# Performance work log

Hardware: AMD Instinct MI355X
Metric: run time of the kernel (lower is better)

The kernel has to match this reference:

```python
import jax, jax.numpy as jnp
import numpy as np

B, L, C, P, H = 1, 1024, 384, 128, 12
SQK, SV, PQK, PV = 16, 16, 4, 8
DIST_EPS = 1e-8


def setup_inputs() -> dict:
    key = jax.random.key(0)
    ks = jax.random.split(key, 16)
    f32 = jnp.float32
    inputs_1d = jax.random.normal(ks[0], (B, L, C), dtype=f32)
    inputs_2d = jax.random.normal(ks[1], (B, L, L, P), dtype=f32)
    # valid rotation matrices from random unit quaternions
    q = jax.random.normal(ks[2], (B, L, 4), dtype=f32)
    q = q / jnp.linalg.norm(q, axis=-1, keepdims=True)
    w, x, y, z = q[..., 0], q[..., 1], q[..., 2], q[..., 3]
    rotations = jnp.stack([
        jnp.stack([1 - 2 * (y * y + z * z), 2 * (x * y - w * z), 2 * (x * z + w * y)], -1),
        jnp.stack([2 * (x * y + w * z), 1 - 2 * (x * x + z * z), 2 * (y * z - w * x)], -1),
        jnp.stack([2 * (x * z - w * y), 2 * (y * z + w * x), 1 - 2 * (x * x + y * y)], -1)], -2)
    translations = jax.random.normal(ks[3], (B, L, 3), dtype=f32)
    mask = jnp.ones((B, L), dtype=bool)
    s = 0.02  # init scale
    tpw_init = float(np.log(np.exp(1.0) - 1.0))  # softplus^{-1}(1)
    return {
        'inputs_1d': inputs_1d, 'inputs_2d': inputs_2d,
        'rotations': rotations, 'translations': translations, 'mask': mask,
        'Wq': jax.random.normal(ks[4], (C, H * SQK), f32) * s, 'bq': jnp.zeros((H * SQK,), f32),
        'Wkv': jax.random.normal(ks[5], (C, H * (SQK + SV)), f32) * s, 'bkv': jnp.zeros((H * (SQK + SV),), f32),
        'Wqp': jax.random.normal(ks[6], (C, 3 * H * PQK), f32) * s, 'bqp': jnp.zeros((3 * H * PQK,), f32),
        'Wkvp': jax.random.normal(ks[7], (C, 3 * H * (PQK + PV)), f32) * s, 'bkvp': jnp.zeros((3 * H * (PQK + PV),), f32),
        'Wpair': jax.random.normal(ks[8], (P, H), f32) * s, 'bpair': jnp.zeros((H,), f32),
        'tpw': jnp.full((H,), tpw_init, f32),
        'Wout': jax.random.normal(ks[9], (H * (SV + P + PV * 4), C), f32) * s, 'bout': jnp.zeros((C,), f32),
    }


def reference(inputs_1d, inputs_2d, rotations, translations, mask,
              Wq, bq, Wkv, bkv, Wqp, bqp, Wkvp, bkvp, Wpair, bpair, tpw, Wout, bout):
    b, l, _ = inputs_1d.shape
    scalar_w = np.sqrt(1.0 / (3 * SQK))
    point_wc = np.sqrt(1.0 / (3 * PQK * 9.0 / 2))
    pair_w = np.sqrt(1.0 / 3)

    # scalar q/k/v: [b,h,l,c]
    q_s = (inputs_1d @ Wq + bq).reshape(b, l, H, SQK).transpose(0, 2, 1, 3)
    kv_s = (inputs_1d @ Wkv + bkv).reshape(b, l, H, SQK + SV).transpose(0, 2, 1, 3)
    k_s, v_s = kv_s[..., :SQK], kv_s[..., SQK:]
    logits = jnp.einsum('bhic,bhjc->bhij', q_s * scalar_w, k_s)

    def apply_rigid(pts):  # pts: [b,l,n,3] local -> global
        return jnp.einsum('blxy,blny->blnx', rotations, pts) + translations[:, :, None, :]

    # point q/k/v; layout '(r n)' -> [b,l,n,3]
    qp = (inputs_1d @ Wqp + bqp).reshape(b, l, 3, H * PQK).transpose(0, 1, 3, 2)
    qp = apply_rigid(qp).reshape(b, l, H, PQK, 3)  # [b,i,h,n,r]
    kvp = (inputs_1d @ Wkvp + bkvp).reshape(b, l, 3, H * (PQK + PV)).transpose(0, 1, 3, 2)
    kvp = apply_rigid(kvp).reshape(b, l, H, PQK + PV, 3)
    kp, vp = kvp[..., :PQK, :], kvp[..., PQK:, :]

    # squared distances via |q|^2 + |k|^2 - 2 q.k (avoids [b,i,j,h,n,r] blowup)
    qk = jnp.einsum('bihnr,bjhnr->bhij', qp, kp)
    sq_q = jnp.sum(qp * qp, (3, 4)).transpose(0, 2, 1)  # [b,h,i]
    sq_k = jnp.sum(kp * kp, (3, 4)).transpose(0, 2, 1)  # [b,h,j]
    dist2 = sq_q[..., :, None] + sq_k[..., None, :] - 2.0 * qk
    pw = -0.5 * point_wc * jax.nn.softplus(tpw)  # [h]
    logits = logits + pw[None, :, None, None] * dist2

    logits = logits + pair_w * (inputs_2d @ Wpair + bpair).transpose(0, 3, 1, 2)

    m2 = mask[:, None, :, None] & mask[:, None, None, :]  # [b,1,i,j]
    logits = jnp.where(m2, logits, jnp.finfo(logits.dtype).min)
    attn = jax.nn.softmax(logits, axis=-1)

    r_s = jnp.einsum('bhij,bhjc->bihc', attn, v_s).reshape(b, l, H * SV)
    r_p = jnp.einsum('bhij,bjhnr->bihnr', attn, vp).reshape(b, l, H * PV, 3)
    # inverse rigid: R^T (p - t)
    loc = jnp.einsum('blyx,blny->blnx', rotations, r_p - translations[:, :, None, :])
    f_p = loc.transpose(0, 1, 3, 2).reshape(b, l, 3 * H * PV)  # '(r n)' layout
    f_n = jnp.sqrt(jnp.sum(loc * loc, -1) + DIST_EPS)  # [b,l,H*PV]
    r_2d = jnp.einsum('bhij,bijc->bihc', attn, inputs_2d).reshape(b, l, H * P)

    final = jnp.concatenate([r_s, f_p, f_n, r_2d], axis=-1)
    return final @ Wout + bout
```

## Files before the change

### kernel.cpp

```cpp
#include <hip/hip_runtime.h>


#define LL 1024
#define CC 384
#define HH 12
#define PP 128
#define NCH 5
#define CHJ 205

static constexpr float SCALAR_W = 0.14433756729740643f;
static constexpr float POINT_WC = 0.1360827634879543f;
static constexpr float PAIR_W   = 0.5773502691896258f;
static constexpr float LOG2E    = 1.4426950408889634f;

#define OFF_IN1D   16
#define OFF_ROT    393232
#define OFF_TRANS  402448
#define OFF_WQ     405520
#define OFF_BQ     479248
#define OFF_WKV    479440
#define OFF_BKV    626896
#define OFF_WQP    627280
#define OFF_BQP    682576
#define OFF_WKVP   682720
#define OFF_BKVP   848608
#define OFF_WPAIR  849040
#define OFF_BPAIR  850576
#define OFF_TPW    850588
#define OFF_WOUT   850600
#define OFF_BOUT   1661608
#define OFF_PROJ   1662000
#define OFF_QPACK  2841648
#define OFF_KPACK  3234864
#define OFF_FIN    4217904

__device__ __forceinline__ float fromlo(unsigned int v) {
    unsigned int a = v << 16; float f; __builtin_memcpy(&f, &a, 4); return f;
}
__device__ __forceinline__ float fromhi(unsigned int v) {
    unsigned int a = v & 0xffff0000u; float f; __builtin_memcpy(&f, &a, 4); return f;
}
__device__ __forceinline__ unsigned short f2bf(float f) {
    unsigned int u; __builtin_memcpy(&u, &f, 4);
    unsigned int lsb = (u >> 16) & 1u;
    u += 0x7fffu + lsb;
    return (unsigned short)(u >> 16);
}
__device__ __forceinline__ float red16(float v) {
    v += __shfl_xor(v, 1);
    v += __shfl_xor(v, 2);
    v += __shfl_xor(v, 4);
    v += __shfl_xor(v, 8);
    return v;
}

__global__ __launch_bounds__(256) void k_detect(const unsigned short* __restrict__ in1d,
                                                int* __restrict__ flag) {
    __shared__ int f;
    if (threadIdx.x == 0) f = 0;
    __syncthreads();
    unsigned short u = in1d[threadIdx.x * 2];
    if ((u & 0x7FFF) >= 0x5000) atomicOr(&f, 1);
    __syncthreads();
    if (threadIdx.x == 0) flag[0] = f;
}

struct CvtArgs { const void* src[16]; int n[16]; int off[16]; };

__global__ __launch_bounds__(256) void k_cvt(CvtArgs a, float* __restrict__ ws) {
    int which = blockIdx.y;
    int n = a.n[which];
    int i4 = (blockIdx.x * 256 + threadIdx.x) * 4;
    if (i4 >= n) return;
    bool f32 = ((const int*)ws)[0] != 0;
    float4 o;
    if (f32) {
        o = *(const float4*)((const float*)a.src[which] + i4);
    } else {
        uint2 u = *(const uint2*)((const unsigned short*)a.src[which] + i4);
        o.x = fromlo(u.x); o.y = fromhi(u.x); o.z = fromlo(u.y); o.w = fromhi(u.y);
    }
    *(float4*)(ws + a.off[which] + i4) = o;
}

__global__ __launch_bounds__(256) void k_proj(const float* __restrict__ A,
                                              const float* __restrict__ W,
                                              const float* __restrict__ bias,
                                              float* __restrict__ proj,
                                              int N, int colOff) {
    __shared__ float lA[4][CC];
    int t = threadIdx.x;
    int row0 = blockIdx.x * 4;
    for (int e = 0; e < 6; ++e) {
        int idx = e * 256 + t;
        int r = idx / CC, k = idx - r * CC;
        lA[r][k] = A[(size_t)(row0 + r) * CC + k];
    }
    __syncthreads();
    int r = t >> 6;
    int c = (t & 63) + blockIdx.y * 64;
    if (c < N) {
        float acc = bias[c];
        const float* wc = W + c;
#pragma unroll 8
        for (int k = 0; k < CC; ++k) acc = fmaf(lA[r][k], wc[(size_t)k * N], acc);
        proj[(size_t)(row0 + r) * 1152 + colOff + c] = acc;
    }
}

__global__ __launch_bounds__(192) void k_pack(const float* __restrict__ proj,
                                              const float* __restrict__ rot,
                                              const float* __restrict__ trans,
                                              const float* __restrict__ tpw,
                                              const float* __restrict__ bpair,
                                              float* __restrict__ Qpack,
                                              float* __restrict__ Kpack) {
    int l = blockIdx.x;
    int t = threadIdx.x;
    int h = t >> 4, lane = t & 15;
    const float* pr = proj + (size_t)l * 1152;

    float R[3][3], tv[3];
#pragma unroll
    for (int x = 0; x < 3; ++x) {
#pragma unroll
        for (int y = 0; y < 3; ++y) R[x][y] = rot[(size_t)l * 9 + x * 3 + y];
        tv[x] = trans[(size_t)l * 3 + x];
    }
    float sp = log1pf(expf(tpw[h]));
    float pw = -0.5f * POINT_WC * sp;

    size_t qb = ((size_t)l * HH + h) * 32;
    size_t kb = ((size_t)l * HH + h) * 80;

    Qpack[qb + lane] = LOG2E * SCALAR_W * pr[h * 16 + lane];
    Kpack[kb + lane * 4 + 0] = pr[192 + h * 32 + lane];
    Kpack[kb + lane * 4 + 1] = pr[192 + h * 32 + 16 + lane];
    if (lane >= 12) Kpack[kb + lane * 4 + 2] = 0.f;

    float tq = 0.f, sqq_p = 0.f;
    if (lane < 12) {
        int p = lane / 3, x = lane - p * 3;
        int n = h * 4 + p;
        float r0 = pr[576 + n], r1 = pr[576 + 48 + n], r2 = pr[576 + 96 + n];
        tq = fmaf(R[x][0], r0, fmaf(R[x][1], r1, fmaf(R[x][2], r2, tv[x])));
        sqq_p = tq * tq;
    }
    float sqq = red16(sqq_p);
    if (lane < 12) Qpack[qb + 16 + lane] = LOG2E * (-2.f * pw) * tq;
    if (lane == 0) Qpack[qb + 28] = LOG2E * (pw * sqq + PAIR_W * bpair[h]);

    float sqk_p = 0.f;
#pragma unroll
    for (int e = 0; e < 3; ++e) {
        int m = e * 16 + lane;
        if (m < 36) {
            int jj = m / 3, x = m - jj * 3;
            int mp = h * 12 + jj;
            float p0 = pr[720 + mp], p1 = pr[720 + 144 + mp], p2 = pr[720 + 288 + mp];
            float tk = fmaf(R[x][0], p0, fmaf(R[x][1], p1, fmaf(R[x][2], p2, tv[x])));
            if (jj < 4) {
                Kpack[kb + (jj * 3 + x) * 4 + 2] = tk;
                sqk_p += tk * tk;
            } else {
                int g = (jj - 4) * 3 + x;
                if (g < 16) Kpack[kb + g * 4 + 3] = tk;
                else        Kpack[kb + 64 + (g - 16)] = tk;
            }
        }
    }
    float sqk = red16(sqk_p);
    if (lane >= 8) Kpack[kb + 64 + lane] = (lane == 13) ? LOG2E * pw * sqk : 0.f;
}

__global__ __launch_bounds__(960) void k_attn(const void* __restrict__ in2d,
                                              const float* __restrict__ rot,
                                              const float* __restrict__ trans,
                                              const float* __restrict__ Wpairf,
                                              const float* __restrict__ Qpack,
                                              const float* __restrict__ Kpack,
                                              const int* __restrict__ flagp,
                                              float* __restrict__ fin) {
    int i = blockIdx.x;
    int t = threadIdx.x;
    int c = t / 192;
    int w = t - c * 192;
    int h = w >> 4, lane = w & 15;
    bool f32m = (*flagp != 0);

    size_t qb = ((size_t)i * HH + h) * 32;
    float qv  = Qpack[qb + lane];
    float qpv = (lane < 12) ? Qpack[qb + 16 + lane] : 0.f;
    float cb  = Qpack[qb + 28];
    float laneC = (lane == 14) ? cb : 0.f;
    float wp[8];
#pragma unroll
    for (int k = 0; k < 8; ++k)
        wp[k] = LOG2E * PAIR_W * Wpairf[(size_t)(lane * 8 + k) * HH + h];

    float S = 0.f, avs = 0.f, aA = 0.f, aB = 0.f;
    float r2[8] = {0.f, 0.f, 0.f, 0.f, 0.f, 0.f, 0.f, 0.f};

    const unsigned short* p2b = (const unsigned short*)in2d + (size_t)i * LL * PP + lane * 8;
    const float*          p2f = (const float*)in2d          + (size_t)i * LL * PP + lane * 8;

    int j0 = c * CHJ;
    int j1 = j0 + CHJ; if (j1 > LL) j1 = LL;

#pragma unroll 2
    for (int j = j0; j < j1; ++j) {
        const float* kbp = Kpack + ((size_t)j * HH + h) * 80;
        float4 kq  = *(const float4*)(kbp + (lane << 2));
        float ex2  = kbp[64 + lane];
        float kv    = kq.x;
        float vv    = kq.y;
        float kpv   = (lane < 12) ? kq.z : 0.f;
        float vA    = kq.w;
        float extra = (lane == 13) ? ex2 : laneC;
        float vB    = ex2;

        float x0, x1, x2, x3, x4, x5, x6, x7;
        if (f32m) {
            float4 a = *(const float4*)(p2f + (size_t)j * PP);
            float4 b = *(const float4*)(p2f + (size_t)j * PP + 4);
            x0 = a.x; x1 = a.y; x2 = a.z; x3 = a.w;
            x4 = b.x; x5 = b.y; x6 = b.z; x7 = b.w;
        } else {
            uint4 u = *(const uint4*)(p2b + (size_t)j * PP);
            x0 = fromlo(u.x); x1 = fromhi(u.x);
            x2 = fromlo(u.y); x3 = fromhi(u.y);
            x4 = fromlo(u.z); x5 = fromhi(u.z);
            x6 = fromlo(u.w); x7 = fromhi(u.w);
        }

        float part = fmaf(qv, kv, fmaf(qpv, kpv, extra));
        part = fmaf(wp[0], x0, part); part = fmaf(wp[1], x1, part);
        part = fmaf(wp[2], x2, part); part = fmaf(wp[3], x3, part);
        part = fmaf(wp[4], x4, part); part = fmaf(wp[5], x5, part);
        part = fmaf(wp[6], x6, part); part = fmaf(wp[7], x7, part);
        part = red16(part);

        float wgt = exp2f(part);
        S += wgt;
        avs = fmaf(wgt, vv, avs);
        aA  = fmaf(wgt, vA, aA);
        aB  = fmaf(wgt, vB, aB);
        r2[0] = fmaf(wgt, x0, r2[0]); r2[1] = fmaf(wgt, x1, r2[1]);
        r2[2] = fmaf(wgt, x2, r2[2]); r2[3] = fmaf(wgt, x3, r2[3]);
        r2[4] = fmaf(wgt, x4, r2[4]); r2[5] = fmaf(wgt, x5, r2[5]);
        r2[6] = fmaf(wgt, x6, r2[6]); r2[7] = fmaf(wgt, x7, r2[7]);
    }

    __shared__ float ldsA[NCH][HH][44];
    __shared__ float ldsR[NCH][HH][PP];
    ldsA[c][h][lane] = avs;
    ldsA[c][h][16 + lane] = aA;
    if (lane < 8) ldsA[c][h][32 + lane] = aB;
    if (lane == 0) ldsA[c][h][40] = S;
#pragma unroll
    for (int e = 0; e < 8; ++e) ldsR[c][h][lane * 8 + e] = r2[e];
    __syncthreads();
    if (c != 0) return;

    float Sv = 0.f, A = 0.f, Pv = 0.f, Bv = 0.f;
    float rr[8] = {0.f, 0.f, 0.f, 0.f, 0.f, 0.f, 0.f, 0.f};
#pragma unroll
    for (int cc = 0; cc < NCH; ++cc) {
        Sv += ldsA[cc][h][40];
        A  += ldsA[cc][h][lane];
        Pv += ldsA[cc][h][16 + lane];
        Bv += ldsA[cc][h][32 + (lane & 7)];
#pragma unroll
        for (int e = 0; e < 8; ++e) rr[e] += ldsR[cc][h][lane * 8 + e];
    }
    float inv = 1.0f / Sv;
    float* fb = fin + (size_t)i * 2112;

    fb[h * 16 + lane] = A * inv;

    __shared__ float lrp[HH * 24];
    lrp[h * 24 + lane] = Pv * inv;
    if (lane < 8) lrp[h * 24 + 16 + lane] = Bv * inv;
    if (lane < 8) {
        float R[3][3], tv[3];
#pragma unroll
        for (int x = 0; x < 3; ++x) {
#pragma unroll
            for (int y = 0; y < 3; ++y) R[x][y] = rot[(size_t)i * 9 + x * 3 + y];
            tv[x] = trans[(size_t)i * 3 + x];
        }
        int m = lane;
        float ry0 = lrp[h * 24 + m * 3 + 0] - tv[0];
        float ry1 = lrp[h * 24 + m * 3 + 1] - tv[1];
        float ry2 = lrp[h * 24 + m * 3 + 2] - tv[2];
        float l0 = fmaf(R[0][0], ry0, fmaf(R[1][0], ry1, R[2][0] * ry2));
        float l1 = fmaf(R[0][1], ry0, fmaf(R[1][1], ry1, R[2][1] * ry2));
        float l2 = fmaf(R[0][2], ry0, fmaf(R[1][2], ry1, R[2][2] * ry2));
        fb[192 +       h * 8 + m] = l0;
        fb[192 +  96 + h * 8 + m] = l1;
        fb[192 + 192 + h * 8 + m] = l2;
        fb[480 + h * 8 + m] = sqrtf(fmaf(l0, l0, fmaf(l1, l1, fmaf(l2, l2, 1e-8f))));
    }

    float4 ra = {rr[0] * inv, rr[1] * inv, rr[2] * inv, rr[3] * inv};
    float4 rb = {rr[4] * inv, rr[5] * inv, rr[6] * inv, rr[7] * inv};
    *(float4*)(fb + 576 + h * PP + lane * 8)     = ra;
    *(float4*)(fb + 576 + h * PP + lane * 8 + 4) = rb;
}

__global__ __launch_bounds__(384) void k_out(const float* __restrict__ fin,
                                             const float* __restrict__ Wf,
                                             const float* __restrict__ boutf,
                                             void* __restrict__ out,
                                             const int* __restrict__ flagp) {
    __shared__ float lA[4 * 2112];
    int t = threadIdx.x;
    int l0 = blockIdx.x * 4;
    for (int e = 0; e < 22; ++e) {
        int idx = e * 384 + t;
        int r = idx / 2112, k = idx - r * 2112;
        lA[idx] = fin[(size_t)(l0 + r) * 2112 + k];
    }
    __syncthreads();
    int r = t / 96, g = t - r * 96;
    int c0 = g * 4;
    const float* lrow = lA + r * 2112;
    float a0 = 0.f, a1 = 0.f, a2 = 0.f, a3 = 0.f;
#pragma unroll 8
    for (int k = 0; k < 2112; ++k) {
        float a = lrow[k];
        float4 w = *(const float4*)(Wf + (size_t)k * CC + c0);
        a0 = fmaf(a, w.x, a0); a1 = fmaf(a, w.y, a1);
        a2 = fmaf(a, w.z, a2); a3 = fmaf(a, w.w, a3);
    }
    a0 += boutf[c0]; a1 += boutf[c0 + 1]; a2 += boutf[c0 + 2]; a3 += boutf[c0 + 3];
    size_t base = (size_t)(l0 + r) * CC + c0;
    if (*flagp != 0) {
        float4 o = {a0, a1, a2, a3};
        *(float4*)((float*)out + base) = o;
    } else {
        ushort4 o = {f2bf(a0), f2bf(a1), f2bf(a2), f2bf(a3)};
        *(ushort4*)((unsigned short*)out + base) = o;
    }
}

extern "C" void kernel_launch(void* const* d_in, const int* in_sizes, int n_in,
                              void* d_out, int out_size, void* d_ws, size_t ws_size,
                              hipStream_t stream) {
    float* ws = (float*)d_ws;
    int* flag = (int*)d_ws;

    k_detect<<<1, 256, 0, stream>>>((const unsigned short*)d_in[0], flag);

    CvtArgs a;
    const int srcIdx[16] = {0, 2, 3, 5, 7, 9, 11, 13, 6, 8, 10, 12, 14, 15, 16, 17};
    const int ns[16]     = {393216, 9216, 3072, 73728, 147456, 55296, 165888, 1536,
                            192, 384, 144, 432, 12, 12, 811008, 384};
    const int offs[16]   = {OFF_IN1D, OFF_ROT, OFF_TRANS, OFF_WQ, OFF_WKV, OFF_WQP,
                            OFF_WKVP, OFF_WPAIR, OFF_BQ, OFF_BKV, OFF_BQP, OFF_BKVP,
                            OFF_BPAIR, OFF_TPW, OFF_WOUT, OFF_BOUT};
    for (int i = 0; i < 16; ++i) { a.src[i] = d_in[srcIdx[i]]; a.n[i] = ns[i]; a.off[i] = offs[i]; }
    k_cvt<<<dim3(792, 16), 256, 0, stream>>>(a, ws);

    float* in1d  = ws + OFF_IN1D;
    float* proj  = ws + OFF_PROJ;
    k_proj<<<dim3(256, 3), 256, 0, stream>>>(in1d, ws + OFF_WQ,   ws + OFF_BQ,   proj, 192, 0);
    k_proj<<<dim3(256, 6), 256, 0, stream>>>(in1d, ws + OFF_WKV,  ws + OFF_BKV,  proj, 384, 192);
    k_proj<<<dim3(256, 3), 256, 0, stream>>>(in1d, ws + OFF_WQP,  ws + OFF_BQP,  proj, 144, 576);
    k_proj<<<dim3(256, 7), 256, 0, stream>>>(in1d, ws + OFF_WKVP, ws + OFF_BKVP, proj, 432, 720);
    k_pack<<<1024, 192, 0, stream>>>(proj, ws + OFF_ROT, ws + OFF_TRANS,
                                     ws + OFF_TPW, ws + OFF_BPAIR,
                                     ws + OFF_QPACK, ws + OFF_KPACK);
    k_attn<<<1024, 960, 0, stream>>>(d_in[1], ws + OFF_ROT, ws + OFF_TRANS,
                                     ws + OFF_WPAIR, ws + OFF_QPACK, ws + OFF_KPACK,
                                     flag, ws + OFF_FIN);
    k_out<<<256, 384, 0, stream>>>(ws + OFF_FIN, ws + OFF_WOUT, ws + OFF_BOUT,
                                   d_out, flag);
}
```

Before: 1.263 ms.

## Prefetch K and pair rows, use DPP reduction, repack Kpack with stride 96

Restructures the attention inner loop in three ways. It software-prefetches the next iteration's Kpack and inputs_2d values before computing the current one, and splits the fp32 and bf16 input paths into separate loops. It replaces the shuffle-based 16-lane reduction with DPP row operations and reorders the FMAs into a tree for shorter dependency chains. Kpack is repacked to a 96-float stride so the extra terms load as one float2, and the per-query constant is dropped, which softmax normalisation cancels. The new launch bound of (960, 8) may squeeze the register budget enough to cause spills.

```diff
diff --git a/kernel.cpp b/kernel.cpp
--- a/kernel.cpp
+++ b/kernel.cpp
@@ -7,6 +7,7 @@
 #define PP 128
 #define NCH 5
 #define CHJ 205
+#define KQSTR (HH * 96)
 
 static constexpr float SCALAR_W = 0.14433756729740643f;
 static constexpr float POINT_WC = 0.1360827634879543f;
@@ -32,7 +33,7 @@
 #define OFF_PROJ   1662000
 #define OFF_QPACK  2841648
 #define OFF_KPACK  3234864
-#define OFF_FIN    4217904
+#define OFF_FIN    4414512
 
 __device__ __forceinline__ float fromlo(unsigned int v) {
     unsigned int a = v << 16; float f; __builtin_memcpy(&f, &a, 4); return f;
@@ -51,6 +52,18 @@
     v += __shfl_xor(v, 2);
     v += __shfl_xor(v, 4);
     v += __shfl_xor(v, 8);
+    return v;
+}
+__device__ __forceinline__ float red16dpp(float v) {
+    int a;
+    a = __float_as_int(v);
+    v += __int_as_float(__builtin_amdgcn_update_dpp(0, a, 0xB1, 0xF, 0xF, true));
+    a = __float_as_int(v);
+    v += __int_as_float(__builtin_amdgcn_update_dpp(0, a, 0x4E, 0xF, 0xF, true));
+    a = __float_as_int(v);
+    v += __int_as_float(__builtin_amdgcn_update_dpp(0, a, 0x141, 0xF, 0xF, true));
+    a = __float_as_int(v);
+    v += __int_as_float(__builtin_amdgcn_update_dpp(0, a, 0x140, 0xF, 0xF, true));
     return v;
 }
 
@@ -131,7 +144,7 @@
     float pw = -0.5f * POINT_WC * sp;
 
     size_t qb = ((size_t)l * HH + h) * 32;
-    size_t kb = ((size_t)l * HH + h) * 80;
+    size_t kb = ((size_t)l * HH + h) * 96;
 
     Qpack[qb + lane] = LOG2E * SCALAR_W * pr[h * 16 + lane];
     Kpack[kb + lane * 4 + 0] = pr[192 + h * 32 + lane];
@@ -165,22 +178,46 @@
             } else {
                 int g = (jj - 4) * 3 + x;
                 if (g < 16) Kpack[kb + g * 4 + 3] = tk;
-                else        Kpack[kb + 64 + (g - 16)] = tk;
+                else        Kpack[kb + 64 + 2 * (g - 16) + 1] = tk;
             }
         }
     }
     float sqk = red16(sqk_p);
-    if (lane >= 8) Kpack[kb + 64 + lane] = (lane == 13) ? LOG2E * pw * sqk : 0.f;
-}
-
-__global__ __launch_bounds__(960) void k_attn(const void* __restrict__ in2d,
-                                              const float* __restrict__ rot,
-                                              const float* __restrict__ trans,
-                                              const float* __restrict__ Wpairf,
-                                              const float* __restrict__ Qpack,
-                                              const float* __restrict__ Kpack,
-                                              const int* __restrict__ flagp,
-                                              float* __restrict__ fin) {
+    if (lane == 0) Kpack[kb + 64] = LOG2E * pw * sqk;
+    if (lane > 0)  Kpack[kb + 64 + 2 * lane] = 0.f;
+    if (lane >= 8) Kpack[kb + 64 + 2 * lane + 1] = 0.f;
+}
+
+#define ABODY(KQ, EXX, EXY, X0, X1, X2, X3, X4, X5, X6, X7)            \
+    {                                                                  \
+        float t0 = fmaf(qv, (KQ).x, (EXX));                            \
+        t0 = fmaf(wp[0], (X0), t0);                                    \
+        float t1 = fmaf(wp[1], (X1), qpv * (KQ).z);                    \
+        t1 = fmaf(wp[2], (X2), t1);                                    \
+        float t2 = fmaf(wp[4], (X4), wp[3] * (X3));                    \
+        float t3 = fmaf(wp[6], (X6), wp[5] * (X5));                    \
+        t3 = fmaf(wp[7], (X7), t3);                                    \
+        float part = (t0 + t1) + (t2 + t3);                            \
+        part = red16dpp(part);                                         \
+        float wgt = exp2f(part);                                       \
+        S += wgt;                                                      \
+        avs = fmaf(wgt, (KQ).y, avs);                                  \
+        aA  = fmaf(wgt, (KQ).w, aA);                                   \
+        aB  = fmaf(wgt, (EXY), aB);                                    \
+        r2[0] = fmaf(wgt, (X0), r2[0]); r2[1] = fmaf(wgt, (X1), r2[1]); \
+        r2[2] = fmaf(wgt, (X2), r2[2]); r2[3] = fmaf(wgt, (X3), r2[3]); \
+        r2[4] = fmaf(wgt, (X4), r2[4]); r2[5] = fmaf(wgt, (X5), r2[5]); \
+        r2[6] = fmaf(wgt, (X6), r2[6]); r2[7] = fmaf(wgt, (X7), r2[7]); \
+    }
+
+__global__ __launch_bounds__(960, 8) void k_attn(const void* __restrict__ in2d,
+                                                 const float* __restrict__ rot,
+                                                 const float* __restrict__ trans,
+                                                 const float* __restrict__ Wpairf,
+                                                 const float* __restrict__ Qpack,
+                                                 const float* __restrict__ Kpack,
+                                                 const int* __restrict__ flagp,
+                                                 float* __restrict__ fin) {
     int i = blockIdx.x;
     int t = threadIdx.x;
     int c = t / 192;
@@ -191,8 +228,6 @@
     size_t qb = ((size_t)i * HH + h) * 32;
     float qv  = Qpack[qb + lane];
     float qpv = (lane < 12) ? Qpack[qb + 16 + lane] : 0.f;
-    float cb  = Qpack[qb + 28];
-    float laneC = (lane == 14) ? cb : 0.f;
     float wp[8];
 #pragma unroll
     for (int k = 0; k < 8; ++k)
@@ -201,54 +236,49 @@
     float S = 0.f, avs = 0.f, aA = 0.f, aB = 0.f;
     float r2[8] = {0.f, 0.f, 0.f, 0.f, 0.f, 0.f, 0.f, 0.f};
 
-    const unsigned short* p2b = (const unsigned short*)in2d + (size_t)i * LL * PP + lane * 8;
-    const float*          p2f = (const float*)in2d          + (size_t)i * LL * PP + lane * 8;
-
     int j0 = c * CHJ;
     int j1 = j0 + CHJ; if (j1 > LL) j1 = LL;
 
-#pragma unroll 2
-    for (int j = j0; j < j1; ++j) {
-        const float* kbp = Kpack + ((size_t)j * HH + h) * 80;
-        float4 kq  = *(const float4*)(kbp + (lane << 2));
-        float ex2  = kbp[64 + lane];
-        float kv    = kq.x;
-        float vv    = kq.y;
-        float kpv   = (lane < 12) ? kq.z : 0.f;
-        float vA    = kq.w;
-        float extra = (lane == 13) ? ex2 : laneC;
-        float vB    = ex2;
-
-        float x0, x1, x2, x3, x4, x5, x6, x7;
-        if (f32m) {
-            float4 a = *(const float4*)(p2f + (size_t)j * PP);
-            float4 b = *(const float4*)(p2f + (size_t)j * PP + 4);
-            x0 = a.x; x1 = a.y; x2 = a.z; x3 = a.w;
-            x4 = b.x; x5 = b.y; x6 = b.z; x7 = b.w;
-        } else {
-            uint4 u = *(const uint4*)(p2b + (size_t)j * PP);
-            x0 = fromlo(u.x); x1 = fromhi(u.x);
-            x2 = fromlo(u.y); x3 = fromhi(u.y);
-            x4 = fromlo(u.z); x5 = fromhi(u.z);
-            x6 = fromlo(u.w); x7 = fromhi(u.w);
+    int koff = (j0 * HH + h) * 96 + (lane << 2);
+    int eoff = (j0 * HH + h) * 96 + 64 + (lane << 1);
+    const unsigned short* xb = (const unsigned short*)in2d + (size_t)i * LL * PP;
+    const float*          xf = (const float*)in2d          + (size_t)i * LL * PP;
+    int xoff = j0 * PP + lane * 8;
+
+    if (!f32m) {
+        float4 kq = *(const float4*)(Kpack + koff);
+        float2 ex = *(const float2*)(Kpack + eoff);
+        uint4  u  = *(const uint4*)(xb + xoff);
+#pragma unroll 1
+        for (int j = j0; j + 1 < j1; ++j) {
+            koff += KQSTR; eoff += KQSTR; xoff += PP;
+            float4 kqn = *(const float4*)(Kpack + koff);
+            float2 exn = *(const float2*)(Kpack + eoff);
+            uint4  un  = *(const uint4*)(xb + xoff);
+            float x0 = fromlo(u.x), x1 = fromhi(u.x);
+            float x2 = fromlo(u.y), x3 = fromhi(u.y);
+            float x4 = fromlo(u.z), x5 = fromhi(u.z);
+            float x6 = fromlo(u.w), x7 = fromhi(u.w);
+            ABODY(kq, ex.x, ex.y, x0, x1, x2, x3, x4, x5, x6, x7);
+            kq = kqn; ex = exn; u = un;
         }
-
-        float part = fmaf(qv, kv, fmaf(qpv, kpv, extra));
-        part = fmaf(wp[0], x0, part); part = fmaf(wp[1], x1, part);
-        part = fmaf(wp[2], x2, part); part = fmaf(wp[3], x3, part);
-        part = fmaf(wp[4], x4, part); part = fmaf(wp[5], x5, part);
-        part = fmaf(wp[6], x6, part); part = fmaf(wp[7], x7, part);
-        part = red16(part);
-
-        float wgt = exp2f(part);
-        S += wgt;
-        avs = fmaf(wgt, vv, avs);
-        aA  = fmaf(wgt, vA, aA);
-        aB  = fmaf(wgt, vB, aB);
-        r2[0] = fmaf(wgt, x0, r2[0]); r2[1] = fmaf(wgt, x1, r2[1]);
-        r2[2] = fmaf(wgt, x2, r2[2]); r2[3] = fmaf(wgt, x3, r2[3]);
-        r2[4] = fmaf(wgt, x4, r2[4]); r2[5] = fmaf(wgt, x5, r2[5]);
-        r2[6] = fmaf(wgt, x6, r2[6]); r2[7] = fmaf(wgt, x7, r2[7]);
+        {
+            float x0 = fromlo(u.x), x1 = fromhi(u.x);
+            float x2 = fromlo(u.y), x3 = fromhi(u.y);
+            float x4 = fromlo(u.z), x5 = fromhi(u.z);
+            float x6 = fromlo(u.w), x7 = fromhi(u.w);
+            ABODY(kq, ex.x, ex.y, x0, x1, x2, x3, x4, x5, x6, x7);
+        }
+    } else {
+#pragma unroll 1
+        for (int j = j0; j < j1; ++j) {
+            float4 kq = *(const float4*)(Kpack + koff);
+            float2 ex = *(const float2*)(Kpack + eoff);
+            float4 a = *(const float4*)(xf + xoff);
+            float4 b = *(const float4*)(xf + xoff + 4);
+            ABODY(kq, ex.x, ex.y, a.x, a.y, a.z, a.w, b.x, b.y, b.z, b.w);
+            koff += KQSTR; eoff += KQSTR; xoff += PP;
+        }
     }
 
     __shared__ float ldsA[NCH][HH][44];
```

Result: slower. 1.310 ms (+3.7%).
